# Kernel tuning notes

Measured on AMD Instinct MI355X. Metric: run time of the kernel, lower is better.

The kernel has to match this reference:

```python
import jax, jax.numpy as jnp
import numpy as np

N, T, D_IN, D_OUT = 131072, 16, 128, 128


def setup_inputs() -> dict:
    key = jax.random.key(0)
    k1, k2, k3, k4 = jax.random.split(key, 4)
    x = jax.random.normal(k1, (N, D_IN), dtype=jnp.float32)
    # sorted type ids, matching HeteroLinear(is_sorted=True)
    type_vec = jnp.sort(jax.random.randint(k2, (N,), 0, T)).astype(jnp.int32)
    # HeteroLinear weight: [num_types, in_channels, out_channels]; out = x @ W[t] + b[t]
    weight = (jax.random.normal(k3, (T, D_IN, D_OUT), dtype=jnp.float32)
              / np.float32(np.sqrt(D_IN)))
    bias = jax.random.normal(k4, (T, D_OUT), dtype=jnp.float32) * 0.01
    return {"x": x, "type_vec": type_vec, "weight": weight, "bias": bias}


def _grouped_matmul(x, weight, type_vec):
    """Segment (grouped) matmul: rows are sorted by type; row i uses weight[type_vec[i]]."""
    try:
        # Native grouped-GEMM primitive (exploits is_sorted=True contiguity).
        group_sizes = jnp.bincount(type_vec, length=weight.shape[0]).astype(jnp.int32)
        return jax.lax.ragged_dot(x, weight, group_sizes)
    except Exception:
        # Fallback: small fixed loop over the T types, masked accumulate.
        out = jnp.zeros((x.shape[0], weight.shape[-1]), dtype=x.dtype)
        for t in range(weight.shape[0]):
            out = out + jnp.where((type_vec == t)[:, None], x @ weight[t], jnp.zeros((), x.dtype))
        return out


def reference(x, type_vec, weight, bias):
    # ToHeteroLinear.fused_forward == HeteroLinear(x, type_vec):
    #   out[i] = x[i] @ weight[type_vec[i]] + bias[type_vec[i]]
    out = _grouped_matmul(x, weight, type_vec)  # [N, D_OUT]
    return out + bias[type_vec]
```

## Files before the change

kernel.cpp:

```cpp
#include <hip/hip_runtime.h>

#define BM  64
#define DD  128
#define LDA 136
#define LDB 136

typedef __bf16 bf16x8 __attribute__((ext_vector_type(8)));
typedef float  f32x4  __attribute__((ext_vector_type(4)));

__device__ __forceinline__ unsigned short f2bf(float f) {
    union { float f; unsigned int u; } c; c.f = f;
    unsigned int u = c.u;
    u += 0x7fffu + ((u >> 16) & 1u);
    return (unsigned short)(u >> 16);
}

__global__ __launch_bounds__(256, 3) void hetero_lin_kernel(
    const float* __restrict__ x,
    const int*   __restrict__ tv,
    const float* __restrict__ w,
    const float* __restrict__ bias,
    float*       __restrict__ out,
    int nrows)
{
    __shared__ unsigned short As[BM * LDA];
    __shared__ unsigned short Bs[DD * LDB];

    const int tid  = threadIdx.x;
    const int row0 = blockIdx.x * BM;

    const int t0 = tv[row0];
    const int t1 = tv[row0 + BM - 1];
    const bool uniform = (t0 == t1);

    {
        const float4* xg = (const float4*)(x + (size_t)row0 * DD);
        #pragma unroll
        for (int i = 0; i < 8; ++i) {
            int f  = tid + i * 256;
            int r  = f >> 5;
            int c4 = (f & 31) << 2;
            float4 v = xg[f];
            ushort4 pk;
            pk.x = f2bf(v.x); pk.y = f2bf(v.y); pk.z = f2bf(v.z); pk.w = f2bf(v.w);
            *(ushort4*)&As[r * LDA + c4] = pk;
        }
    }

    const int wave = tid >> 6;
    const int lane = tid & 63;
    const int q    = lane >> 4;
    const int n16  = lane & 15;
    const int k0l = (tid & 31) << 2;
    const int ng  = tid >> 5;

    for (int t = t0; t <= t1; ++t) {
        if (t > t0) __syncthreads();

        {
            const float* wt = w + (size_t)t * DD * DD;
            #pragma unroll
            for (int i = 0; i < 4; ++i) {
                int n0 = (ng + (i << 3)) << 2;
                float4 r0 = *(const float4*)&wt[(k0l + 0) * DD + n0];
                float4 r1 = *(const float4*)&wt[(k0l + 1) * DD + n0];
                float4 r2 = *(const float4*)&wt[(k0l + 2) * DD + n0];
                float4 r3 = *(const float4*)&wt[(k0l + 3) * DD + n0];
                ushort4 c0, c1, c2, c3;
                c0.x=f2bf(r0.x); c0.y=f2bf(r1.x); c0.z=f2bf(r2.x); c0.w=f2bf(r3.x);
                c1.x=f2bf(r0.y); c1.y=f2bf(r1.y); c1.z=f2bf(r2.y); c1.w=f2bf(r3.y);
                c2.x=f2bf(r0.z); c2.y=f2bf(r1.z); c2.z=f2bf(r2.z); c2.w=f2bf(r3.z);
                c3.x=f2bf(r0.w); c3.y=f2bf(r1.w); c3.z=f2bf(r2.w); c3.w=f2bf(r3.w);
                *(ushort4*)&Bs[(n0 + 0) * LDB + k0l] = c0;
                *(ushort4*)&Bs[(n0 + 1) * LDB + k0l] = c1;
                *(ushort4*)&Bs[(n0 + 2) * LDB + k0l] = c2;
                *(ushort4*)&Bs[(n0 + 3) * LDB + k0l] = c3;
            }
        }
        __syncthreads();

        f32x4 acc[8];
        #pragma unroll
        for (int nt = 0; nt < 8; ++nt) acc[nt] = (f32x4){0.f, 0.f, 0.f, 0.f};

        const unsigned short* arow = &As[(wave * 16 + n16) * LDA];
        #pragma unroll
        for (int kk = 0; kk < 4; ++kk) {
            bf16x8 a = *(const bf16x8*)&arow[kk * 32 + q * 8];
            #pragma unroll
            for (int nt = 0; nt < 8; ++nt) {
                bf16x8 b = *(const bf16x8*)&Bs[(nt * 16 + n16) * LDB + kk * 32 + q * 8];
                acc[nt] = __builtin_amdgcn_mfma_f32_16x16x32_bf16(a, b, acc[nt], 0, 0, 0);
            }
        }

        const int rbase = row0 + wave * 16 + q * 4;
        bool m0 = true, m1 = true, m2 = true, m3 = true;
        if (!uniform) {
            m0 = (tv[rbase + 0] == t);
            m1 = (tv[rbase + 1] == t);
            m2 = (tv[rbase + 2] == t);
            m3 = (tv[rbase + 3] == t);
        }
        #pragma unroll
        for (int nt = 0; nt < 8; ++nt) {
            int col  = nt * 16 + n16;
            float bv = bias[t * DD + col];
            float* o = out + (size_t)rbase * DD + col;
            if (m0) o[0 * DD] = acc[nt][0] + bv;
            if (m1) o[1 * DD] = acc[nt][1] + bv;
            if (m2) o[2 * DD] = acc[nt][2] + bv;
            if (m3) o[3 * DD] = acc[nt][3] + bv;
        }
    }
}

extern "C" void kernel_launch(void* const* d_in, const int* in_sizes, int n_in,
                              void* d_out, int out_size, void* d_ws, size_t ws_size,
                              hipStream_t stream) {
    const float* x    = (const float*)d_in[0];
    const int*   tv   = (const int*)d_in[1];
    const float* w    = (const float*)d_in[2];
    const float* bias = (const float*)d_in[3];
    float*       out  = (float*)d_out;
    int nrows = in_sizes[0] / DD;
    int grid  = nrows / BM;
    hipLaunchKernelGGL(hetero_lin_kernel, dim3(grid), dim3(256), 0, stream,
                       x, tv, w, bias, out, nrows);
}
```

Measured before the change: 141.9 us.

## Pre-transpose weights to bf16 in workspace and drop LDS staging in main kernel

A small prologue kernel converts each type's weight matrix to bf16 and transposes it into workspace once per call. The main kernel then keeps its 16 x rows in registers as MFMA B operands, reads weight fragments directly from global/L2, and swaps operand roles so each lane writes contiguous float4 output per row. This removes the per-block LDS fill, fp32-to-bf16 conversion of weights and the block-wide barriers, and decides type segments per wave rather than per block. In exchange it adds a second kernel launch and repeated global/L2 reads of the weight fragments by every wave.

```diff
diff --git a/kernel.cpp b/kernel.cpp
--- a/kernel.cpp
+++ b/kernel.cpp
@@ -1,9 +1,8 @@
 #include <hip/hip_runtime.h>
 
-#define BM  64
-#define DD  128
-#define LDA 136
-#define LDB 136
+#define DD 128
+#define BM 64
+#define T_TYPES 16
 
 typedef __bf16 bf16x8 __attribute__((ext_vector_type(8)));
 typedef float  f32x4  __attribute__((ext_vector_type(4)));
@@ -15,102 +14,105 @@
     return (unsigned short)(u >> 16);
 }
 
-__global__ __launch_bounds__(256, 3) void hetero_lin_kernel(
+__global__ __launch_bounds__(256) void transpose_w_kernel(
+    const float* __restrict__ w, unsigned short* __restrict__ wbf)
+{
+    __shared__ float lds[DD * 33];
+    const int t   = blockIdx.x >> 2;
+    const int m0  = (blockIdx.x & 3) * 32;
+    const int tid = threadIdx.x;
+    const float* wt = w + (size_t)t * DD * DD;
+
+    #pragma unroll
+    for (int i = 0; i < 4; ++i) {
+        int f = tid + i * 256;
+        int k = f >> 3;
+        int c = (f & 7) * 4;
+        float4 v = *(const float4*)&wt[k * DD + m0 + c];
+        lds[k * 33 + c + 0] = v.x;
+        lds[k * 33 + c + 1] = v.y;
+        lds[k * 33 + c + 2] = v.z;
+        lds[k * 33 + c + 3] = v.w;
+    }
+    __syncthreads();
+    #pragma unroll
+    for (int i = 0; i < 4; ++i) {
+        int g  = tid + i * 256;
+        int ml = g >> 5;
+        int k4 = (g & 31) * 4;
+        ushort4 o;
+        o.x = f2bf(lds[(k4 + 0) * 33 + ml]);
+        o.y = f2bf(lds[(k4 + 1) * 33 + ml]);
+        o.z = f2bf(lds[(k4 + 2) * 33 + ml]);
+        o.w = f2bf(lds[(k4 + 3) * 33 + ml]);
+        *(ushort4*)&wbf[((size_t)t * DD + m0 + ml) * DD + k4] = o;
+    }
+}
+
+__global__ __launch_bounds__(256, 4) void hetero_main_kernel(
     const float* __restrict__ x,
     const int*   __restrict__ tv,
-    const float* __restrict__ w,
+    const __bf16* __restrict__ wbf,
     const float* __restrict__ bias,
-    float*       __restrict__ out,
-    int nrows)
+    float*       __restrict__ out)
 {
-    __shared__ unsigned short As[BM * LDA];
-    __shared__ unsigned short Bs[DD * LDB];
+    const int tid   = threadIdx.x;
+    const int wave  = tid >> 6;
+    const int lane  = tid & 63;
+    const int q     = lane >> 4;
+    const int n16   = lane & 15;
+    const int wrow0 = blockIdx.x * BM + wave * 16;
+    const int grow  = wrow0 + n16;
 
-    const int tid  = threadIdx.x;
-    const int row0 = blockIdx.x * BM;
+    const int t0 = tv[wrow0];
+    const int t1 = tv[wrow0 + 15];
 
-    const int t0 = tv[row0];
-    const int t1 = tv[row0 + BM - 1];
-    const bool uniform = (t0 == t1);
-
+    bf16x8 xb[4];
     {
-        const float4* xg = (const float4*)(x + (size_t)row0 * DD);
+        const float* xr = x + (size_t)grow * DD;
         #pragma unroll
-        for (int i = 0; i < 8; ++i) {
-            int f  = tid + i * 256;
-            int r  = f >> 5;
-            int c4 = (f & 31) << 2;
-            float4 v = xg[f];
-            ushort4 pk;
-            pk.x = f2bf(v.x); pk.y = f2bf(v.y); pk.z = f2bf(v.z); pk.w = f2bf(v.w);
-            *(ushort4*)&As[r * LDA + c4] = pk;
+        for (int kk = 0; kk < 4; ++kk) {
+            float4 v0 = *(const float4*)&xr[kk * 32 + q * 8];
+            float4 v1 = *(const float4*)&xr[kk * 32 + q * 8 + 4];
+            bf16x8 b;
+            b[0] = (__bf16)v0.x; b[1] = (__bf16)v0.y;
+            b[2] = (__bf16)v0.z; b[3] = (__bf16)v0.w;
+            b[4] = (__bf16)v1.x; b[5] = (__bf16)v1.y;
+            b[6] = (__bf16)v1.z; b[7] = (__bf16)v1.w;
+            xb[kk] = b;
         }
     }
 
-    const int wave = tid >> 6;
-    const int lane = tid & 63;
-    const int q    = lane >> 4;
-    const int n16  = lane & 15;
-    const int k0l = (tid & 31) << 2;
-    const int ng  = tid >> 5;
+    const int myt = (t0 == t1) ? t0 : tv[grow];
 
     for (int t = t0; t <= t1; ++t) {
-        if (t > t0) __syncthreads();
-
-        {
-            const float* wt = w + (size_t)t * DD * DD;
-            #pragma unroll
-            for (int i = 0; i < 4; ++i) {
-                int n0 = (ng + (i << 3)) << 2;
-                float4 r0 = *(const float4*)&wt[(k0l + 0) * DD + n0];
-                float4 r1 = *(const float4*)&wt[(k0l + 1) * DD + n0];
-                float4 r2 = *(const float4*)&wt[(k0l + 2) * DD + n0];
-                float4 r3 = *(const float4*)&wt[(k0l + 3) * DD + n0];
-                ushort4 c0, c1, c2, c3;
-                c0.x=f2bf(r0.x); c0.y=f2bf(r1.x); c0.z=f2bf(r2.x); c0.w=f2bf(r3.x);
-                c1.x=f2bf(r0.y); c1.y=f2bf(r1.y); c1.z=f2bf(r2.y); c1.w=f2bf(r3.y);
-                c2.x=f2bf(r0.z); c2.y=f2bf(r1.z); c2.z=f2bf(r2.z); c2.w=f2bf(r3.z);
-                c3.x=f2bf(r0.w); c3.y=f2bf(r1.w); c3.z=f2bf(r2.w); c3.w=f2bf(r3.w);
-                *(ushort4*)&Bs[(n0 + 0) * LDB + k0l] = c0;
-                *(ushort4*)&Bs[(n0 + 1) * LDB + k0l] = c1;
-                *(ushort4*)&Bs[(n0 + 2) * LDB + k0l] = c2;
-                *(ushort4*)&Bs[(n0 + 3) * LDB + k0l] = c3;
-            }
-        }
-        __syncthreads();
-
         f32x4 acc[8];
         #pragma unroll
-        for (int nt = 0; nt < 8; ++nt) acc[nt] = (f32x4){0.f, 0.f, 0.f, 0.f};
+        for (int mt = 0; mt < 8; ++mt) acc[mt] = (f32x4){0.f, 0.f, 0.f, 0.f};
 
-        const unsigned short* arow = &As[(wave * 16 + n16) * LDA];
+        const __bf16* wt = wbf + (size_t)t * DD * DD;
         #pragma unroll
         for (int kk = 0; kk < 4; ++kk) {
-            bf16x8 a = *(const bf16x8*)&arow[kk * 32 + q * 8];
             #pragma unroll
-            for (int nt = 0; nt < 8; ++nt) {
-                bf16x8 b = *(const bf16x8*)&Bs[(nt * 16 + n16) * LDB + kk * 32 + q * 8];
-                acc[nt] = __builtin_amdgcn_mfma_f32_16x16x32_bf16(a, b, acc[nt], 0, 0, 0);
+            for (int mt = 0; mt < 8; ++mt) {
+                bf16x8 a = *(const bf16x8*)&wt[(mt * 16 + n16) * DD + kk * 32 + q * 8];
+                acc[mt] = __builtin_amdgcn_mfma_f32_16x16x32_bf16(a, xb[kk], acc[mt], 0, 0, 0);
             }
         }
 
-        const int rbase = row0 + wave * 16 + q * 4;
-        bool m0 = true, m1 = true, m2 = true, m3 = true;
-        if (!uniform) {
-            m0 = (tv[rbase + 0] == t);
-            m1 = (tv[rbase + 1] == t);
-            m2 = (tv[rbase + 2] == t);
-            m3 = (tv[rbase + 3] == t);
-        }
+        const bool st = (myt == t);
+        float* orow = out + (size_t)grow * DD;
         #pragma unroll
-        for (int nt = 0; nt < 8; ++nt) {
-            int col  = nt * 16 + n16;
-            float bv = bias[t * DD + col];
-            float* o = out + (size_t)rbase * DD + col;
-            if (m0) o[0 * DD] = acc[nt][0] + bv;
-            if (m1) o[1 * DD] = acc[nt][1] + bv;
-            if (m2) o[2 * DD] = acc[nt][2] + bv;
-            if (m3) o[3 * DD] = acc[nt][3] + bv;
+        for (int mt = 0; mt < 8; ++mt) {
+            float4 bv = *(const float4*)&bias[t * DD + mt * 16 + q * 4];
+            if (st) {
+                float4 r;
+                r.x = acc[mt][0] + bv.x;
+                r.y = acc[mt][1] + bv.y;
+                r.z = acc[mt][2] + bv.z;
+                r.w = acc[mt][3] + bv.w;
+                *(float4*)&orow[mt * 16 + q * 4] = r;
+            }
         }
     }
 }
@@ -123,8 +125,13 @@
     const float* w    = (const float*)d_in[2];
     const float* bias = (const float*)d_in[3];
     float*       out  = (float*)d_out;
+    unsigned short* wbf = (unsigned short*)d_ws;
+
     int nrows = in_sizes[0] / DD;
     int grid  = nrows / BM;
-    hipLaunchKernelGGL(hetero_lin_kernel, dim3(grid), dim3(256), 0, stream,
-                       x, tv, w, bias, out, nrows);
+
+    hipLaunchKernelGGL(transpose_w_kernel, dim3(T_TYPES * 4), dim3(256), 0, stream,
+                       w, wbf);
+    hipLaunchKernelGGL(hetero_main_kernel, dim3(grid), dim3(256), 0, stream,
+                       x, tv, (const __bf16*)wbf, bias, out);
 }
```

New measurement: 146.6 us. 1.03x slower.

## Pre-pack weights into MFMA fragment layout in a prep kernel, read B from global

Applied to the files above, without the earlier changes.

Adds a small prep kernel that converts each type's weight matrix to bf16 in the exact per-lane MFMA B-fragment order and stores it in workspace. The main kernel then loads B fragments straight from global/L2 instead of having every block convert and transpose 64KB of fp32 weights into shared memory. A-tile LDS is XOR-swizzled without padding and A fragments are held in registers, which cuts LDS use and allows higher occupancy (launch bounds raised to 4). The cost is an extra kernel launch and B reads from cache per wave instead of from LDS.

```diff
diff --git a/kernel.cpp b/kernel.cpp
--- a/kernel.cpp
+++ b/kernel.cpp
@@ -1,32 +1,68 @@
 #include <hip/hip_runtime.h>
 
-#define BM  64
-#define DD  128
-#define LDA 136
-#define LDB 136
+#define DD 128
+#define BM 64
+#define T_TYPES 16
 
 typedef __bf16 bf16x8 __attribute__((ext_vector_type(8)));
+typedef __bf16 bf16x4 __attribute__((ext_vector_type(4)));
 typedef float  f32x4  __attribute__((ext_vector_type(4)));
 
-__device__ __forceinline__ unsigned short f2bf(float f) {
-    union { float f; unsigned int u; } c; c.f = f;
-    unsigned int u = c.u;
-    u += 0x7fffu + ((u >> 16) & 1u);
-    return (unsigned short)(u >> 16);
+__global__ __launch_bounds__(256) void transpose_w_frag_kernel(
+    const float* __restrict__ w, unsigned short* __restrict__ wbf)
+{
+    __shared__ float lds[DD * 33];
+    const int t   = blockIdx.x >> 2;
+    const int n0  = (blockIdx.x & 3) * 32;
+    const int tid = threadIdx.x;
+    const float* wt = w + (size_t)t * DD * DD;
+
+    #pragma unroll
+    for (int i = 0; i < 4; ++i) {
+        int f = tid + i * 256;
+        int k = f >> 3;
+        int c = (f & 7) * 4;
+        float4 v = *(const float4*)&wt[k * DD + n0 + c];
+        lds[k * 33 + c + 0] = v.x;
+        lds[k * 33 + c + 1] = v.y;
+        lds[k * 33 + c + 2] = v.z;
+        lds[k * 33 + c + 3] = v.w;
+    }
+    __syncthreads();
+    #pragma unroll
+    for (int i = 0; i < 4; ++i) {
+        int g  = tid + i * 256;
+        int nl = g >> 5;
+        int k4 = (g & 31) * 4;
+        int n  = n0 + nl;
+        int nt  = n >> 4, n16 = n & 15;
+        int kk  = k4 >> 5, q = (k4 >> 3) & 3, jb = k4 & 7;
+        int lane = q * 16 + n16;
+        size_t ofs = ((((size_t)t * 8 + nt) * 4 + kk) * 64 + lane) * 8 + jb;
+        ushort4 o;
+        union { __bf16 b; unsigned short u; } cv;
+        cv.b = (__bf16)lds[(k4 + 0) * 33 + nl]; o.x = cv.u;
+        cv.b = (__bf16)lds[(k4 + 1) * 33 + nl]; o.y = cv.u;
+        cv.b = (__bf16)lds[(k4 + 2) * 33 + nl]; o.z = cv.u;
+        cv.b = (__bf16)lds[(k4 + 3) * 33 + nl]; o.w = cv.u;
+        *(ushort4*)&wbf[ofs] = o;
+    }
 }
 
-__global__ __launch_bounds__(256, 3) void hetero_lin_kernel(
+__global__ __launch_bounds__(256, 4) void hetero_main_kernel(
     const float* __restrict__ x,
     const int*   __restrict__ tv,
-    const float* __restrict__ w,
+    const __bf16* __restrict__ wbf,
     const float* __restrict__ bias,
-    float*       __restrict__ out,
-    int nrows)
+    float*       __restrict__ out)
 {
-    __shared__ unsigned short As[BM * LDA];
-    __shared__ unsigned short Bs[DD * LDB];
+    __shared__ __bf16 As[BM * DD];
 
     const int tid  = threadIdx.x;
+    const int wave = tid >> 6;
+    const int lane = tid & 63;
+    const int q    = lane >> 4;
+    const int n16  = lane & 15;
     const int row0 = blockIdx.x * BM;
 
     const int t0 = tv[row0];
@@ -41,56 +77,37 @@
             int r  = f >> 5;
             int c4 = (f & 31) << 2;
             float4 v = xg[f];
-            ushort4 pk;
-            pk.x = f2bf(v.x); pk.y = f2bf(v.y); pk.z = f2bf(v.z); pk.w = f2bf(v.w);
-            *(ushort4*)&As[r * LDA + c4] = pk;
+            bf16x4 pk;
+            pk[0] = (__bf16)v.x; pk[1] = (__bf16)v.y;
+            pk[2] = (__bf16)v.z; pk[3] = (__bf16)v.w;
+            int g = c4 >> 3;
+            *(bf16x4*)&As[r * DD + ((g ^ (r & 7)) << 3) + (c4 & 7)] = pk;
+        }
+    }
+    __syncthreads();
+
+    bf16x8 a[4];
+    {
+        const __bf16* arow = &As[(wave * 16 + n16) * DD];
+        #pragma unroll
+        for (int kk = 0; kk < 4; ++kk) {
+            int gr = ((kk << 2) | q) ^ (n16 & 7);
+            a[kk] = *(const bf16x8*)&arow[gr << 3];
         }
     }
 
-    const int wave = tid >> 6;
-    const int lane = tid & 63;
-    const int q    = lane >> 4;
-    const int n16  = lane & 15;
-    const int k0l = (tid & 31) << 2;
-    const int ng  = tid >> 5;
-
     for (int t = t0; t <= t1; ++t) {
-        if (t > t0) __syncthreads();
-
-        {
-            const float* wt = w + (size_t)t * DD * DD;
-            #pragma unroll
-            for (int i = 0; i < 4; ++i) {
-                int n0 = (ng + (i << 3)) << 2;
-                float4 r0 = *(const float4*)&wt[(k0l + 0) * DD + n0];
-                float4 r1 = *(const float4*)&wt[(k0l + 1) * DD + n0];
-                float4 r2 = *(const float4*)&wt[(k0l + 2) * DD + n0];
-                float4 r3 = *(const float4*)&wt[(k0l + 3) * DD + n0];
-                ushort4 c0, c1, c2, c3;
-                c0.x=f2bf(r0.x); c0.y=f2bf(r1.x); c0.z=f2bf(r2.x); c0.w=f2bf(r3.x);
-                c1.x=f2bf(r0.y); c1.y=f2bf(r1.y); c1.z=f2bf(r2.y); c1.w=f2bf(r3.y);
-                c2.x=f2bf(r0.z); c2.y=f2bf(r1.z); c2.z=f2bf(r2.z); c2.w=f2bf(r3.z);
-                c3.x=f2bf(r0.w); c3.y=f2bf(r1.w); c3.z=f2bf(r2.w); c3.w=f2bf(r3.w);
-                *(ushort4*)&Bs[(n0 + 0) * LDB + k0l] = c0;
-                *(ushort4*)&Bs[(n0 + 1) * LDB + k0l] = c1;
-                *(ushort4*)&Bs[(n0 + 2) * LDB + k0l] = c2;
-                *(ushort4*)&Bs[(n0 + 3) * LDB + k0l] = c3;
-            }
-        }
-        __syncthreads();
-
         f32x4 acc[8];
         #pragma unroll
         for (int nt = 0; nt < 8; ++nt) acc[nt] = (f32x4){0.f, 0.f, 0.f, 0.f};
 
-        const unsigned short* arow = &As[(wave * 16 + n16) * LDA];
+        const __bf16* wt = wbf + ((size_t)t * 32) * 512;
         #pragma unroll
-        for (int kk = 0; kk < 4; ++kk) {
-            bf16x8 a = *(const bf16x8*)&arow[kk * 32 + q * 8];
+        for (int nt = 0; nt < 8; ++nt) {
             #pragma unroll
-            for (int nt = 0; nt < 8; ++nt) {
-                bf16x8 b = *(const bf16x8*)&Bs[(nt * 16 + n16) * LDB + kk * 32 + q * 8];
-                acc[nt] = __builtin_amdgcn_mfma_f32_16x16x32_bf16(a, b, acc[nt], 0, 0, 0);
+            for (int kk = 0; kk < 4; ++kk) {
+                bf16x8 b = *(const bf16x8*)&wt[(((nt << 2) | kk) << 9) + (lane << 3)];
+                acc[nt] = __builtin_amdgcn_mfma_f32_16x16x32_bf16(a[kk], b, acc[nt], 0, 0, 0);
             }
         }
 
@@ -104,9 +121,9 @@
         }
         #pragma unroll
         for (int nt = 0; nt < 8; ++nt) {
-            int col  = nt * 16 + n16;
-            float bv = bias[t * DD + col];
-            float* o = out + (size_t)rbase * DD + col;
+            int   col = nt * 16 + n16;
+            float bv  = bias[t * DD + col];
+            float* o  = out + (size_t)rbase * DD + col;
             if (m0) o[0 * DD] = acc[nt][0] + bv;
             if (m1) o[1 * DD] = acc[nt][1] + bv;
             if (m2) o[2 * DD] = acc[nt][2] + bv;
@@ -123,8 +140,13 @@
     const float* w    = (const float*)d_in[2];
     const float* bias = (const float*)d_in[3];
     float*       out  = (float*)d_out;
+    unsigned short* wbf = (unsigned short*)d_ws;
+
     int nrows = in_sizes[0] / DD;
     int grid  = nrows / BM;
-    hipLaunchKernelGGL(hetero_lin_kernel, dim3(grid), dim3(256), 0, stream,
-                       x, tv, w, bias, out, nrows);
+
+    hipLaunchKernelGGL(transpose_w_frag_kernel, dim3(T_TYPES * 4), dim3(256), 0, stream,
+                       w, wbf);
+    hipLaunchKernelGGL(hetero_main_kernel, dim3(grid), dim3(256), 0, stream,
+                       x, tv, (const __bf16*)wbf, bias, out);
 }
```

Result: faster. 131.6 us (-7.2%).
